# Kernel tuning notes

Hardware: AMD Instinct MI355X
Metric: run time of the kernel (lower is better)

## Reference

```python
import jax, jax.numpy as jnp
import numpy as np

NH = 4  # attention heads

def rmsnorm(x, w, eps=1e-5):
    return x * jax.lax.rsqrt(jnp.mean(x * x, axis=-1, keepdims=True) + eps) * w

def gin(x, src, dst, W, b):
    # GINConv(eps=0): Linear(x + sum_{j->i} x_j)
    agg = jax.ops.segment_sum(x[src], dst, num_segments=x.shape[0])
    return (x + agg) @ W + b

def attn_pool(xb, vt, qkv_w, qkv_b, ao_w, ao_b):
    # xb: [B, Nmax, H] padded nodes (zeros participate, matching the torch code
    # which passes no key_padding_mask); vt: [T, H] virtual tokens.
    B, Nmax, H = xb.shape
    T = vt.shape[0]
    hd = H // NH
    q = (vt @ qkv_w[:, :H] + qkv_b[:H]).reshape(T, NH, hd)
    k = (xb @ qkv_w[:, H:2 * H] + qkv_b[H:2 * H]).reshape(B, Nmax, NH, hd)
    v = (xb @ qkv_w[:, 2 * H:] + qkv_b[2 * H:]).reshape(B, Nmax, NH, hd)
    scores = jnp.einsum('thd,bkhd->bhtk', q, k) / jnp.sqrt(jnp.asarray(hd, xb.dtype))
    attn = jax.nn.softmax(scores, axis=-1)
    o = jnp.einsum('bhtk,bkhd->bthd', attn, v).reshape(B, T, H)
    return o @ ao_w + ao_b

def mamba(tokens, in_w, conv_w, conv_b, x_w, dt_w, dt_b, A_log, D, out_w, norm_w, normf_w):
    # HF MambaModel with num_hidden_layers=1 (slow path), inputs_embeds path.
    B, T, H = tokens.shape
    I, K = conv_w.shape
    S = A_log.shape[1]
    R = dt_w.shape[0]
    res = tokens
    h = rmsnorm(tokens, norm_w)
    proj = h @ in_w                      # [B,T,2I]
    u, gate = jnp.split(proj, 2, axis=-1)
    up = jnp.pad(u, ((0, 0), (K - 1, 0), (0, 0)))  # causal depthwise conv1d
    conv = sum(conv_w[:, k] * up[:, k:k + T, :] for k in range(K)) + conv_b
    u = jax.nn.silu(conv)                # [B,T,I]
    ssm = u @ x_w                        # [B,T,R+2S]
    dtr, Bm, Cm = jnp.split(ssm, [R, R + S], axis=-1)
    dt = jax.nn.softplus(dtr @ dt_w + dt_b)  # [B,T,I]
    A = -jnp.exp(A_log)                  # [I,S]

    def step(hstate, inp):
        dt_t, B_t, C_t, u_t = inp        # [B,I],[B,S],[B,S],[B,I]
        dA = jnp.exp(dt_t[:, :, None] * A)
        dBu = dt_t[:, :, None] * B_t[:, None, :] * u_t[:, :, None]
        hstate = dA * hstate + dBu
        y = jnp.sum(hstate * C_t[:, None, :], axis=-1)
        return hstate, y

    h0 = jnp.zeros((B, I, S), tokens.dtype)
    xs = (dt.transpose(1, 0, 2), Bm.transpose(1, 0, 2), Cm.transpose(1, 0, 2), u.transpose(1, 0, 2))
    _, ys = jax.lax.scan(step, h0, xs)
    y = ys.transpose(1, 0, 2) + u * D
    y = y * jax.nn.silu(gate)
    out = y @ out_w                      # [B,T,H]
    return rmsnorm(res + out, normf_w)

def _forward(x, edge_index, batch, num_graphs, nodes_per_graph,
             w_in, b_in, gin_w, gin_b, vt, qkv_w, qkv_b, ao_w, ao_b,
             m_in_w, m_conv_w, m_conv_b, m_x_w, m_dt_w, m_dt_b,
             m_A_log, m_D, m_out_w, m_norm_w, m_normf_w, w_out, b_out):
    src, dst = edge_index[0], edge_index[1]
    N = x.shape[0]
    starts = jnp.searchsorted(batch, jnp.arange(num_graphs, dtype=batch.dtype))
    pos = jnp.arange(N, dtype=batch.dtype) - starts[batch]
    x = gin(x, src, dst, w_in, b_in)
    H = x.shape[-1]
    for l in range(gin_w.shape[0]):
        g = gin(x, src, dst, gin_w[l], gin_b[l])
        xb = jnp.zeros((num_graphs, nodes_per_graph, H), x.dtype).at[batch, pos].set(x)
        tokens = attn_pool(xb, vt[l], qkv_w[l], qkv_b[l], ao_w[l], ao_b[l])
        gf = mamba(tokens, m_in_w, m_conv_w, m_conv_b, m_x_w, m_dt_w, m_dt_b,
                   m_A_log, m_D, m_out_w, m_norm_w, m_normf_w)
        x = g + gf.mean(axis=1)[batch]
    x = gin(x, src, dst, w_out, b_out)
    return jax.ops.segment_sum(x, batch, num_segments=num_graphs)

def setup_inputs() -> dict:
    key = jax.random.key(0)
    ks = jax.random.split(key, 24)
    N, E, B, NPG = 131072, 2097152, 128, 1024
    IN = H = OUT = 128
    T, L = 8, 2
    I, S, R, K = 256, 16, 8, 4  # mamba: intermediate, state, dt_rank, conv kernel
    w = lambda k, s: (jax.random.normal(k, s, jnp.float32) * 0.02)
    x = jax.random.normal(ks[0], (N, IN), jnp.float32)
    edge_index = jax.random.randint(ks[1], (2, E), 0, N, jnp.int32)
    batch = (jnp.arange(N) // NPG).astype(jnp.int32)
    return dict(
        x=x, edge_index=edge_index, batch=batch, num_graphs=B, nodes_per_graph=NPG,
        w_in=w(ks[2], (IN, H)), b_in=jnp.zeros((H,), jnp.float32),
        gin_w=w(ks[3], (L, H, H)), gin_b=jnp.zeros((L, H), jnp.float32),
        vt=jax.random.normal(ks[4], (L, T, H), jnp.float32),
        qkv_w=w(ks[5], (L, H, 3 * H)), qkv_b=jnp.zeros((L, 3 * H), jnp.float32),
        ao_w=w(ks[6], (L, H, H)), ao_b=jnp.zeros((L, H), jnp.float32),
        m_in_w=w(ks[7], (H, 2 * I)),
        m_conv_w=w(ks[8], (I, K)), m_conv_b=jnp.zeros((I,), jnp.float32),
        m_x_w=w(ks[9], (I, R + 2 * S)),
        m_dt_w=w(ks[10], (R, I)), m_dt_b=jnp.full((I,), 0.1, jnp.float32),
        m_A_log=jnp.log(jnp.tile(jnp.arange(1, S + 1, dtype=jnp.float32), (I, 1))),
        m_D=jnp.ones((I,), jnp.float32),
        m_out_w=w(ks[11], (I, H)),
        m_norm_w=jnp.ones((H,), jnp.float32), m_normf_w=jnp.ones((H,), jnp.float32),
        w_out=w(ks[12], (H, OUT)), b_out=jnp.zeros((OUT,), jnp.float32),
    )

def reference(x, edge_index, batch, num_graphs, nodes_per_graph,
              w_in, b_in, gin_w, gin_b, vt, qkv_w, qkv_b, ao_w, ao_b,
              m_in_w, m_conv_w, m_conv_b, m_x_w, m_dt_w, m_dt_b,
              m_A_log, m_D, m_out_w, m_norm_w, m_normf_w, w_out, b_out):
    return _forward(x, edge_index, batch, num_graphs, nodes_per_graph,
                    w_in, b_in, gin_w, gin_b, vt, qkv_w, qkv_b, ao_w, ao_b,
                    m_in_w, m_conv_w, m_conv_b, m_x_w, m_dt_w, m_dt_b,
                    m_A_log, m_D, m_out_w, m_norm_w, m_normf_w, w_out, b_out)
```

## Files before the change

kernel.cpp:

```cpp
#include <hip/hip_runtime.h>

#define HDIM 128
#define TTOK 8
#define NPG 1024
#define NBUCK 512
#define BSHIFT 8
#define BCAP 5120
#define EPB 4096
#define PARTSZ 4160

typedef unsigned short ushort;
typedef unsigned int uint;
typedef __attribute__((ext_vector_type(8))) short short8;
typedef __attribute__((ext_vector_type(4))) float f32x4;

__device__ __forceinline__ ushort f2bf(float f) {
    unsigned int x = __float_as_uint(f);
    return (ushort)((x + 0x7FFFu + ((x >> 16) & 1u)) >> 16);
}
__device__ __forceinline__ float blo(uint u) { return __uint_as_float(u << 16); }
__device__ __forceinline__ float bhi(uint u) { return __uint_as_float(u & 0xFFFF0000u); }
__device__ __forceinline__ uint pk(float a, float b) {
    return (uint)f2bf(a) | ((uint)f2bf(b) << 16);
}

__global__ __launch_bounds__(256) void bin_kernel(const int* __restrict__ src,
    const int* __restrict__ dst, int mode, int* __restrict__ bcursor,
    uint* __restrict__ pairbuf, int E)
{
    __shared__ int lcnt[NBUCK];
    __shared__ int lbase[NBUCK];
    int tid = threadIdx.x;
    int e0 = blockIdx.x * EPB;
    for (int i = tid; i < NBUCK; i += 256) lcnt[i] = 0;
    __syncthreads();
    uint pkd[16];
    int bk[16], rk[16];
    #pragma unroll
    for (int i = 0; i < 16; ++i) {
        int e = e0 + i * 256 + tid;
        int s = (e < E) ? src[e] : 0;
        int d = (e < E) ? dst[e] : 0;
        int key = mode ? s : d;
        uint pay = mode ? (uint)(d >> 10) : (uint)s;
        if (e >= E) key = -1;
        int b = key >> BSHIFT;
        bk[i] = b;
        pkd[i] = ((uint)(key & 255) << 17) | pay;
        rk[i] = (key >= 0) ? atomicAdd(&lcnt[b], 1) : 0;
    }
    __syncthreads();
    for (int i = tid; i < NBUCK; i += 256) {
        int c = lcnt[i];
        lbase[i] = c ? atomicAdd(&bcursor[i], c) : 0;
    }
    __syncthreads();
    #pragma unroll
    for (int i = 0; i < 16; ++i) {
        if (bk[i] >= 0) {
            int slot = lbase[bk[i]] + rk[i];
            if (slot < BCAP) pairbuf[(size_t)bk[i] * BCAP + slot] = pkd[i];
        }
    }
}

__global__ __launch_bounds__(256) void bucket_sort_kernel(const uint* __restrict__ pairbuf,
    const int* __restrict__ bcount,
    int* __restrict__ ssrc, int* __restrict__ starts, int* __restrict__ countn, int N)
{
    __shared__ int sc[NBUCK];
    __shared__ int lcount[256];
    __shared__ int lcur[256];
    __shared__ int lss[BCAP];
    int b = blockIdx.x;
    int tid = threadIdx.x;
    sc[tid] = min(bcount[tid], BCAP);
    sc[tid + 256] = min(bcount[tid + 256], BCAP);
    lcount[tid] = 0;
    __syncthreads();
    for (int off = 1; off < NBUCK; off <<= 1) {
        int a0 = (tid >= off) ? sc[tid - off] : 0;
        int a1 = (tid + 256 >= off) ? sc[tid + 256 - off] : 0;
        __syncthreads();
        sc[tid] += a0; sc[tid + 256] += a1;
        __syncthreads();
    }
    int nb = min(bcount[b], BCAP);
    int base = sc[b] - nb;
    const uint* pp = pairbuf + (size_t)b * BCAP;
    for (int i = tid; i < nb; i += 256)
        atomicAdd(&lcount[(pp[i] >> 17) & 255], 1);
    __syncthreads();
    int v = lcount[tid];
    lcur[tid] = v;
    __syncthreads();
    for (int off = 1; off < 256; off <<= 1) {
        int t = (tid >= off) ? lcur[tid - off] : 0;
        __syncthreads();
        lcur[tid] += t;
        __syncthreads();
    }
    int excl = lcur[tid] - v;
    int node = b * 256 + tid;
    starts[node] = base + excl;
    countn[node] = v;
    __syncthreads();
    lcur[tid] = excl;
    __syncthreads();
    for (int i = tid; i < nb; i += 256) {
        uint p = pp[i];
        int pos = atomicAdd(&lcur[(p >> 17) & 255], 1);
        lss[pos] = (int)(p & 0x1FFFFu);
    }
    __syncthreads();
    for (int i = tid; i < nb; i += 256) ssrc[base + i] = lss[i];
    if (b == NBUCK - 1 && tid == 0) starts[N] = base + nb;
}

__global__ __launch_bounds__(256) void convert_kernel(const float* __restrict__ in,
                                                      ushort* __restrict__ outb, int n4)
{
    int i = blockIdx.x * 256 + threadIdx.x;
    if (i >= n4) return;
    float4 v = ((const float4*)in)[i];
    uint2 o;
    o.x = pk(v.x, v.y); o.y = pk(v.z, v.w);
    ((uint2*)outb)[i] = o;
}

__global__ __launch_bounds__(512) void gin_fused_kernel(const ushort* __restrict__ XS,
    const int* __restrict__ ssrc, const int* __restrict__ starts,
    const int* __restrict__ count,
    const float* __restrict__ W, const float* __restrict__ bias,
    const float* __restrict__ GF, ushort* __restrict__ XD)
{
    __shared__ ushort Xl[128 * 128];
    __shared__ ushort Wl[128 * 128];
    int tid = threadIdx.x;
    size_t r0 = (size_t)blockIdx.x * 128;
    {
        uint4* wl = (uint4*)Wl;
        for (int i = tid; i < 2048; i += 512) {
            int n = i & 127, c = i >> 7;
            const float* wp = W + (size_t)(c * 8) * 128 + n;
            float w0 = wp[0], w1 = wp[128], w2 = wp[256], w3 = wp[384];
            float w4 = wp[512], w5 = wp[640], w6 = wp[768], w7 = wp[896];
            uint4 u;
            u.x = pk(w0, w1); u.y = pk(w2, w3); u.z = pk(w4, w5); u.w = pk(w6, w7);
            wl[n * 16 + (c ^ (n & 15))] = u;
        }
    }
    {
        int g16 = tid >> 4, lane16 = tid & 15;
        #pragma unroll
        for (int rr = 0; rr < 4; ++rr) {
            int row = g16 * 4 + rr;
            int node = (int)r0 + row;
            uint4 sv = *((const uint4*)(XS + (size_t)node * HDIM) + lane16);
            float a0 = blo(sv.x), a1 = bhi(sv.x), a2 = blo(sv.y), a3 = bhi(sv.y);
            float a4 = blo(sv.z), a5 = bhi(sv.z), a6 = blo(sv.w), a7 = bhi(sv.w);
            int es = starts[node], cn = count[node];
            for (int j0 = 0; j0 < cn; j0 += 16) {
                int myid = (j0 + lane16 < cn) ? ssrc[es + j0 + lane16] : 0;
                int m = min(16, cn - j0);
                int j = 0;
                for (; j + 7 < m; j += 8) {
                    uint4 u[8];
                    #pragma unroll
                    for (int q = 0; q < 8; ++q) {
                        int sidx = __shfl(myid, j + q, 16);
                        u[q] = *((const uint4*)(XS + (size_t)sidx * HDIM) + lane16);
                    }
                    #pragma unroll
                    for (int q = 0; q < 8; ++q) {
                        a0 += blo(u[q].x); a1 += bhi(u[q].x);
                        a2 += blo(u[q].y); a3 += bhi(u[q].y);
                        a4 += blo(u[q].z); a5 += bhi(u[q].z);
                        a6 += blo(u[q].w); a7 += bhi(u[q].w);
                    }
                }
                for (; j + 3 < m; j += 4) {
                    uint4 u[4];
                    #pragma unroll
                    for (int q = 0; q < 4; ++q) {
                        int sidx = __shfl(myid, j + q, 16);
                        u[q] = *((const uint4*)(XS + (size_t)sidx * HDIM) + lane16);
                    }
                    #pragma unroll
                    for (int q = 0; q < 4; ++q) {
                        a0 += blo(u[q].x); a1 += bhi(u[q].x);
                        a2 += blo(u[q].y); a3 += bhi(u[q].y);
                        a4 += blo(u[q].z); a5 += bhi(u[q].z);
                        a6 += blo(u[q].w); a7 += bhi(u[q].w);
                    }
                }
                for (; j < m; ++j) {
                    int sidx = __shfl(myid, j, 16);
                    uint4 ua = *((const uint4*)(XS + (size_t)sidx * HDIM) + lane16);
                    a0 += blo(ua.x); a1 += bhi(ua.x);
                    a2 += blo(ua.y); a3 += bhi(ua.y);
                    a4 += blo(ua.z); a5 += bhi(ua.z);
                    a6 += blo(ua.w); a7 += bhi(ua.w);
                }
            }
            uint4 o;
            o.x = pk(a0, a1); o.y = pk(a2, a3); o.z = pk(a4, a5); o.w = pk(a6, a7);
            ((uint4*)Xl)[row * 16 + (lane16 ^ (row & 15))] = o;
        }
    }
    __syncthreads();
    int wave = tid >> 6;
    int lane = tid & 63;
    int m16 = lane & 15, quad = lane >> 4;
    const short8* Xf = (const short8*)Xl;
    const short8* Wf = (const short8*)Wl;
    short8 afr[4];
    #pragma unroll
    for (int kc = 0; kc < 4; ++kc)
        afr[kc] = Xf[(wave * 16 + m16) * 16 + ((kc * 4 + quad) ^ m16)];
    int graph = (int)(r0 >> 10);
    #pragma unroll
    for (int ct = 0; ct < 8; ++ct) {
        int col = ct * 16 + m16;
        short8 bfr[4];
        #pragma unroll
        for (int kc = 0; kc < 4; ++kc)
            bfr[kc] = Wf[col * 16 + ((kc * 4 + quad) ^ m16)];
        f32x4 acc = {0.f, 0.f, 0.f, 0.f};
        #pragma unroll
        for (int kc = 0; kc < 4; ++kc)
            acc = __builtin_amdgcn_mfma_f32_16x16x32_bf16(afr[kc], bfr[kc], acc, 0, 0, 0);
        float add = bias[col] + (GF ? GF[(size_t)graph * HDIM + col] : 0.f);
        #pragma unroll
        for (int r = 0; r < 4; ++r)
            XD[(r0 + wave * 16 + quad * 4 + r) * HDIM + col] = f2bf(acc[r] + add);
    }
}

__global__ __launch_bounds__(256) void attn_prep_kernel(const float* __restrict__ vt,
    const float* __restrict__ qkv_w, const float* __restrict__ qkv_b, float* __restrict__ P)
{
    __shared__ float vtl[TTOK][HDIM];
    __shared__ float q[TTOK][HDIM];
    int l = blockIdx.x;
    const float* vtp = vt + (size_t)l * TTOK * HDIM;
    const float* qw = qkv_w + (size_t)l * 128 * 384;
    const float* qb = qkv_b + (size_t)l * 384;
    float* Pp = P + (size_t)l * 4 * TTOK * HDIM;
    int tid = threadIdx.x;
    for (int i = tid; i < TTOK * HDIM; i += 256) vtl[i >> 7][i & 127] = vtp[i];
    __syncthreads();
    for (int i = tid; i < TTOK * HDIM; i += 256) {
        int t = i >> 7, j = i & 127;
        float acc = qb[j];
        for (int c = 0; c < 128; ++c) acc += vtl[t][c] * qw[c * 384 + j];
        q[t][j] = acc;
    }
    __syncthreads();
    const float scale = 0.17677669529663687f;
    for (int i = tid; i < 4 * TTOK * HDIM; i += 256) {
        int h = i >> 10, t = (i >> 7) & 7, cc = i & 127;
        float acc = 0.f;
        for (int d = 0; d < 32; ++d)
            acc += qw[cc * 384 + 128 + h * 32 + d] * q[t][h * 32 + d];
        Pp[i] = acc * scale;
    }
}

__global__ __launch_bounds__(256) void attn_part_kernel(const ushort* __restrict__ X,
    const float* __restrict__ P, float* __restrict__ PART)
{
    __shared__ ushort Xl[128 * 128];
    __shared__ float  St[32 * 132];
    __shared__ ushort Pl[32 * 128];
    __shared__ float lm[32], ll[32], lalpha[32];
    int tid = threadIdx.x;
    int bp = blockIdx.x;
    int b = bp >> 2, part = bp & 3;
    int wave = tid >> 6, lane = tid & 63;
    int m16 = lane & 15, quad = lane >> 4;

    for (int i = tid; i < 2048; i += 256) {
        float2 v = *(const float2*)(P + (size_t)i * 2);
        ((uint*)Pl)[i] = pk(v.x, v.y);
    }
    if (tid < 32) { lm[tid] = -1e30f; ll[tid] = 0.f; }
    __syncthreads();
    short8 aP[2][4];
    #pragma unroll
    for (int mt = 0; mt < 2; ++mt)
        #pragma unroll
        for (int kc = 0; kc < 4; ++kc)
            aP[mt][kc] = *(const short8*)&Pl[(mt * 16 + m16) * 128 + (kc * 4 + quad) * 8];
    __syncthreads();

    f32x4 oacc[2][2] = {};
    const uint4* xsg = (const uint4*)(X + (size_t)b * NPG * HDIM);

    for (int t8i = 0; t8i < 2; ++t8i) {
        int t8 = part * 2 + t8i;
        {
            const uint4* xs = xsg + t8 * 2048;
            uint4* xl = (uint4*)Xl;
            for (int i = tid; i < 2048; i += 256) {
                int row = i >> 4, cc = i & 15;
                xl[row * 16 + (cc ^ (row & 15))] = xs[i];
            }
        }
        __syncthreads();
        {
            f32x4 sacc[2][2] = {};
            #pragma unroll
            for (int kc = 0; kc < 4; ++kc) {
                short8 bx[2];
                #pragma unroll
                for (int ntl = 0; ntl < 2; ++ntl) {
                    int node = (2 * wave + ntl) * 16 + m16;
                    bx[ntl] = *(const short8*)&Xl[node * 128 + (((kc * 4 + quad) ^ m16) << 3)];
                }
                #pragma unroll
                for (int mt = 0; mt < 2; ++mt)
                    #pragma unroll
                    for (int ntl = 0; ntl < 2; ++ntl)
                        sacc[mt][ntl] = __builtin_amdgcn_mfma_f32_16x16x32_bf16(
                            aP[mt][kc], bx[ntl], sacc[mt][ntl], 0, 0, 0);
            }
            #pragma unroll
            for (int mt = 0; mt < 2; ++mt)
                #pragma unroll
                for (int ntl = 0; ntl < 2; ++ntl)
                    #pragma unroll
                    for (int r = 0; r < 4; ++r)
                        St[(mt * 16 + quad * 4 + r) * 132 + (2 * wave + ntl) * 16 + m16]
                            = sacc[mt][ntl][r];
        }
        __syncthreads();
        {
            int j = tid >> 3, g = tid & 7;
            const float* rowp = &St[j * 132 + g * 16];
            float4 v0 = *(const float4*)(rowp);
            float4 v1 = *(const float4*)(rowp + 4);
            float4 v2 = *(const float4*)(rowp + 8);
            float4 v3 = *(const float4*)(rowp + 12);
            float mx = fmaxf(fmaxf(fmaxf(v0.x, v0.y), fmaxf(v0.z, v0.w)),
                             fmaxf(fmaxf(v1.x, v1.y), fmaxf(v1.z, v1.w)));
            mx = fmaxf(mx, fmaxf(fmaxf(fmaxf(v2.x, v2.y), fmaxf(v2.z, v2.w)),
                                 fmaxf(fmaxf(v3.x, v3.y), fmaxf(v3.z, v3.w))));
            mx = fmaxf(mx, __shfl_down(mx, 4, 8));
            mx = fmaxf(mx, __shfl_down(mx, 2, 8));
            mx = fmaxf(mx, __shfl_down(mx, 1, 8));
            mx = __shfl(mx, 0, 8);
            float mold = lm[j];
            float Mn = fmaxf(mold, mx);
            float alpha = __expf(mold - Mn);
            float p0 = __expf(v0.x - Mn), p1 = __expf(v0.y - Mn), p2 = __expf(v0.z - Mn), p3 = __expf(v0.w - Mn);
            float p4 = __expf(v1.x - Mn), p5 = __expf(v1.y - Mn), p6 = __expf(v1.z - Mn), p7 = __expf(v1.w - Mn);
            float p8 = __expf(v2.x - Mn), p9 = __expf(v2.y - Mn), pa = __expf(v2.z - Mn), pb = __expf(v2.w - Mn);
            float pc = __expf(v3.x - Mn), pd = __expf(v3.y - Mn), pe = __expf(v3.z - Mn), pf = __expf(v3.w - Mn);
            float s = ((p0 + p1) + (p2 + p3)) + ((p4 + p5) + (p6 + p7))
                    + ((p8 + p9) + (pa + pb)) + ((pc + pd) + (pe + pf));
            s += __shfl_down(s, 4, 8);
            s += __shfl_down(s, 2, 8);
            s += __shfl_down(s, 1, 8);
            if (g == 0) {
                ll[j] = ll[j] * alpha + s;
                lm[j] = Mn;
                lalpha[j] = alpha;
            }
            uint4 u0, u1;
            u0.x = pk(p0, p1); u0.y = pk(p2, p3); u0.z = pk(p4, p5); u0.w = pk(p6, p7);
            u1.x = pk(p8, p9); u1.y = pk(pa, pb); u1.z = pk(pc, pd); u1.w = pk(pe, pf);
            ((uint4*)Pl)[j * 16 + ((2 * g) ^ (j & 15))] = u0;
            ((uint4*)Pl)[j * 16 + ((2 * g + 1) ^ (j & 15))] = u1;
        }
        __syncthreads();
        {
            #pragma unroll
            for (int mt = 0; mt < 2; ++mt)
                #pragma unroll
                for (int r = 0; r < 4; ++r) {
                    float a = lalpha[mt * 16 + quad * 4 + r];
                    oacc[mt][0][r] *= a;
                    oacc[mt][1][r] *= a;
                }
            #pragma unroll
            for (int kc = 0; kc < 4; ++kc) {
                short8 ap2[2], bx[2];
                #pragma unroll
                for (int mt = 0; mt < 2; ++mt)
                    ap2[mt] = *(const short8*)&Pl[(mt * 16 + m16) * 128 + (((kc * 4 + quad) ^ m16) << 3)];
                #pragma unroll
                for (int ntl = 0; ntl < 2; ++ntl) {
                    int cf = (2 * wave + ntl) * 16 + m16;
                    int chi = cf >> 3, clo = cf & 7;
                    short8 v;
                    #pragma unroll
                    for (int jj = 0; jj < 8; ++jj) {
                        int row = kc * 32 + quad * 8 + jj;
                        v[jj] = (short)Xl[(row << 7) + ((chi ^ (row & 15)) << 3) + clo];
                    }
                    bx[ntl] = v;
                }
                #pragma unroll
                for (int mt = 0; mt < 2; ++mt)
                    #pragma unroll
                    for (int ntl = 0; ntl < 2; ++ntl)
                        oacc[mt][ntl] = __builtin_amdgcn_mfma_f32_16x16x32_bf16(
                            ap2[mt], bx[ntl], oacc[mt][ntl], 0, 0, 0);
            }
        }
        __syncthreads();
    }
    float* PB = PART + ((size_t)b * 4 + part) * PARTSZ;
    #pragma unroll
    for (int mt = 0; mt < 2; ++mt)
        #pragma unroll
        for (int r = 0; r < 4; ++r) {
            int j = mt * 16 + quad * 4 + r;
            PB[j * 128 + (2 * wave + 0) * 16 + m16] = oacc[mt][0][r];
            PB[j * 128 + (2 * wave + 1) * 16 + m16] = oacc[mt][1][r];
        }
    if (tid < 32) { PB[4096 + tid] = lm[tid]; PB[4128 + tid] = ll[tid]; }
}

__global__ __launch_bounds__(1024) void mamba_kernel(const float* __restrict__ PART,
    const float* __restrict__ qkv_w, const float* __restrict__ qkv_b,
    const float* __restrict__ ao_w, const float* __restrict__ ao_b,
    const float* __restrict__ in_w, const float* __restrict__ conv_w,
    const float* __restrict__ conv_b, const float* __restrict__ x_w,
    const float* __restrict__ dt_w, const float* __restrict__ dt_b,
    const float* __restrict__ A_log, const float* __restrict__ Dp,
    const float* __restrict__ out_w, const float* __restrict__ norm_w,
    const float* __restrict__ normf_w, float* __restrict__ GF)
{
    constexpr int I = 256, S = 16;
    __shared__ float R[32 * 132];
    __shared__ float wgt[4][32];
    __shared__ float inv[32];
    __shared__ float tok[TTOK][HDIM];
    __shared__ float hn[TTOK][HDIM];
    __shared__ float uu[TTOK][I];
    __shared__ float gg[TTOK][I];
    __shared__ float ssm[TTOK][40];
    __shared__ float yy[TTOK][I];
    int b = blockIdx.x, tid = threadIdx.x;

    const float* PB = PART + (size_t)b * 4 * PARTSZ;
    if (tid < 32) {
        int j = tid;
        float m0 = PB[4096 + j], m1 = PB[PARTSZ + 4096 + j];
        float m2 = PB[2 * PARTSZ + 4096 + j], m3 = PB[3 * PARTSZ + 4096 + j];
        float M = fmaxf(fmaxf(m0, m1), fmaxf(m2, m3));
        float w0 = __expf(m0 - M), w1 = __expf(m1 - M);
        float w2 = __expf(m2 - M), w3 = __expf(m3 - M);
        float L = w0 * PB[4128 + j] + w1 * PB[PARTSZ + 4128 + j]
                + w2 * PB[2 * PARTSZ + 4128 + j] + w3 * PB[3 * PARTSZ + 4128 + j];
        wgt[0][j] = w0; wgt[1][j] = w1; wgt[2][j] = w2; wgt[3][j] = w3;
        inv[j] = 1.f / L;
    }
    __syncthreads();
    #pragma unroll
    for (int it = 0; it < 4; ++it) {
        int idx = it * 1024 + tid;
        int j = idx >> 7, c = idx & 127;
        float v = wgt[0][j] * PB[idx] + wgt[1][j] * PB[PARTSZ + idx]
                + wgt[2][j] * PB[2 * PARTSZ + idx] + wgt[3][j] * PB[3 * PARTSZ + idx];
        R[j * 132 + c] = v * inv[j];
    }
    __syncthreads();
    {
        int t = tid >> 7, col = tid & 127;
        int h = col >> 5;
        const float* rp = &R[(h * 8 + t) * 132];
        const float* wp = qkv_w + 256 + col;
        float acc = qkv_b[256 + col];
        for (int c = 0; c < 128; c += 8) {
            float w[8];
            #pragma unroll
            for (int q = 0; q < 8; ++q) w[q] = wp[(size_t)(c + q) * 384];
            #pragma unroll
            for (int q = 0; q < 8; ++q) acc += rp[c + q] * w[q];
        }
        hn[t][col] = acc;
    }
    __syncthreads();
    {
        int t = tid >> 7, col = tid & 127;
        const float* hp = hn[t];
        const float* wp = ao_w + col;
        float acc = ao_b[col];
        for (int k = 0; k < 128; k += 8) {
            float w[8];
            #pragma unroll
            for (int q = 0; q < 8; ++q) w[q] = wp[(size_t)(k + q) * 128];
            #pragma unroll
            for (int q = 0; q < 8; ++q) acc += hp[k + q] * w[q];
        }
        tok[t][col] = acc;
    }
    __syncthreads();

    if (tid < 512) {
        int t = tid >> 6, lane = tid & 63;
        float v0 = tok[t][lane], v1 = tok[t][lane + 64];
        float s = v0 * v0 + v1 * v1;
        #pragma unroll
        for (int off = 32; off; off >>= 1) s += __shfl_down(s, off);
        s = __shfl(s, 0);
        float r = rsqrtf(s * (1.f / 128.f) + 1e-5f);
        hn[t][lane] = v0 * r * norm_w[lane];
        hn[t][lane + 64] = v1 * r * norm_w[lane + 64];
    }
    __syncthreads();
    {
        int j = tid & 511, tq = tid >> 9;
        float acc[4] = {0.f, 0.f, 0.f, 0.f};
        const float* wp = in_w + j;
        for (int c = 0; c < 128; c += 8) {
            float w[8];
            #pragma unroll
            for (int q = 0; q < 8; ++q) w[q] = wp[(size_t)(c + q) * 512];
            #pragma unroll
            for (int q = 0; q < 8; ++q) {
                float wq = w[q];
                #pragma unroll
                for (int k = 0; k < 4; ++k) acc[k] += hn[tq * 4 + k][c + q] * wq;
            }
        }
        if (j < 256) {
            #pragma unroll
            for (int k = 0; k < 4; ++k) uu[tq * 4 + k][j] = acc[k];
        } else {
            #pragma unroll
            for (int k = 0; k < 4; ++k) gg[tq * 4 + k][j - 256] = acc[k];
        }
    }
    __syncthreads();
    if (tid < 256) {
        int i = tid;
        float cw0 = conv_w[i * 4 + 0], cw1 = conv_w[i * 4 + 1];
        float cw2 = conv_w[i * 4 + 2], cw3 = conv_w[i * 4 + 3];
        float cb = conv_b[i];
        float uv[TTOK];
        #pragma unroll
        for (int t = 0; t < TTOK; ++t) uv[t] = uu[t][i];
        #pragma unroll
        for (int t = 0; t < TTOK; ++t) {
            float a = cw3 * uv[t] + cb;
            if (t >= 1) a += cw2 * uv[t - 1];
            if (t >= 2) a += cw1 * uv[t - 2];
            if (t >= 3) a += cw0 * uv[t - 3];
            float sg = 1.f / (1.f + __expf(-a));
            uu[t][i] = a * sg;
        }
    }
    __syncthreads();
    {
        int t = tid >> 7, j = tid & 127;
        if (j < 40) {
            float acc = 0.f;
            const float* wp = x_w + j;
            const float* up = uu[t];
            for (int c = 0; c < 256; c += 8) {
                float w[8];
                #pragma unroll
                for (int q = 0; q < 8; ++q) w[q] = wp[(size_t)(c + q) * 40];
                #pragma unroll
                for (int q = 0; q < 8; ++q) acc += up[c + q] * w[q];
            }
            ssm[t][j] = acc;
        }
    }
    __syncthreads();
    if (tid < 256) {
        int i = tid;
        float dw[8];
        #pragma unroll
        for (int r = 0; r < 8; ++r) dw[r] = dt_w[r * 256 + i];
        float dtbias = dt_b[i];
        float a[S], st[S];
        #pragma unroll
        for (int s = 0; s < S; ++s) { a[s] = -__expf(A_log[i * S + s]); st[s] = 0.f; }
        float Di = Dp[i];
        for (int t = 0; t < TTOK; ++t) {
            float d = dtbias;
            #pragma unroll
            for (int r = 0; r < 8; ++r) d += ssm[t][r] * dw[r];
            d = (d > 20.f) ? d : log1pf(__expf(d));
            float ut = uu[t][i];
            float du = d * ut;
            float y = 0.f;
            #pragma unroll
            for (int s = 0; s < S; ++s) {
                float dA = __expf(d * a[s]);
                st[s] = dA * st[s] + du * ssm[t][8 + s];
                y += st[s] * ssm[t][24 + s];
            }
            y += ut * Di;
            float g = gg[t][i];
            float sg = 1.f / (1.f + __expf(-g));
            yy[t][i] = y * g * sg;
        }
    }
    __syncthreads();
    {
        int t = tid >> 7, c = tid & 127;
        float acc = tok[t][c];
        const float* wp = out_w + c;
        const float* yp = yy[t];
        for (int i = 0; i < 256; i += 8) {
            float w[8];
            #pragma unroll
            for (int q = 0; q < 8; ++q) w[q] = wp[(size_t)(i + q) * 128];
            #pragma unroll
            for (int q = 0; q < 8; ++q) acc += yp[i + q] * w[q];
        }
        hn[t][c] = acc;
    }
    __syncthreads();
    if (tid < 512) {
        int t = tid >> 6, lane = tid & 63;
        float v0 = hn[t][lane], v1 = hn[t][lane + 64];
        float s = v0 * v0 + v1 * v1;
        #pragma unroll
        for (int off = 32; off; off >>= 1) s += __shfl_down(s, off);
        s = __shfl(s, 0);
        float r = rsqrtf(s * (1.f / 128.f) + 1e-5f);
        hn[t][lane] = v0 * r * normf_w[lane];
        hn[t][lane + 64] = v1 * r * normf_w[lane + 64];
    }
    __syncthreads();
    if (tid < 128) {
        float s = 0.f;
        #pragma unroll
        for (int t = 0; t < TTOK; ++t) s += hn[t][tid];
        GF[(size_t)b * HDIM + tid] = s * (1.f / TTOK);
    }
}

__global__ __launch_bounds__(512) void final_count_kernel(const ushort* __restrict__ X,
    const uint* __restrict__ pairbuf, const int* __restrict__ bcount,
    float* __restrict__ PS2)
{
    __shared__ uint hist[128 * 128];
    __shared__ ushort Xb[256 * 128];
    int bkt = blockIdx.x, tid = threadIdx.x;
    for (int i = tid; i < 16384; i += 512) hist[i] = 0u;
    {
        const uint4* xs = (const uint4*)(X + ((size_t)bkt << 8) * HDIM);
        uint4* xl = (uint4*)Xb;
        for (int i = tid; i < 4096; i += 512) {
            int row = i >> 4, cc = i & 15;
            xl[row * 16 + (cc ^ (row & 15))] = xs[i];
        }
    }
    __syncthreads();
    int nb = min(bcount[bkt], BCAP);
    const uint* pp = pairbuf + (size_t)bkt * BCAP;
    for (int i = tid; i < nb; i += 512) {
        uint p = pp[i];
        int g = (int)(p & 0x1FFFFu);
        int s8 = (int)((p >> 17) & 255);
        atomicAdd(&hist[g * 128 + (s8 >> 1)], 1u << ((s8 & 1) * 16));
    }
    if (tid < 256) {
        int g = bkt >> 2;
        atomicAdd(&hist[g * 128 + (tid >> 1)], 1u << ((tid & 1) * 16));
    }
    __syncthreads();
    for (int i = tid; i < 16384; i += 512) {
        uint u = hist[i];
        hist[i] = pk((float)(u & 0xFFFFu), (float)(u >> 16));
    }
    __syncthreads();
    int wave = tid >> 6, lane = tid & 63;
    int m16 = lane & 15, quad = lane >> 4;
    const short8* Af = (const short8*)hist;
    short8 afr[8];
    #pragma unroll
    for (int kc = 0; kc < 8; ++kc)
        afr[kc] = Af[(wave * 16 + m16) * 32 + kc * 4 + quad];
    float* PBo = PS2 + (size_t)bkt * 16384;
    #pragma unroll
    for (int ct = 0; ct < 8; ++ct) {
        f32x4 acc = {0.f, 0.f, 0.f, 0.f};
        int n = ct * 16 + m16;
        int chi = n >> 3, clo = n & 7;
        #pragma unroll
        for (int kc = 0; kc < 8; ++kc) {
            short8 bx;
            #pragma unroll
            for (int j = 0; j < 8; ++j) {
                int k = kc * 32 + quad * 8 + j;
                bx[j] = (short)Xb[(k << 7) + (((chi) ^ (k & 15)) << 3) + clo];
            }
            acc = __builtin_amdgcn_mfma_f32_16x16x32_bf16(afr[kc], bx, acc, 0, 0, 0);
        }
        #pragma unroll
        for (int r = 0; r < 4; ++r)
            PBo[(wave * 16 + quad * 4 + r) * 128 + n] = acc[r];
    }
}

__global__ __launch_bounds__(128) void final_mm_kernel(const float* __restrict__ PS2,
    const float* __restrict__ w_out, const float* __restrict__ b_out,
    float* __restrict__ out)
{
    __shared__ float Sm[HDIM];
    int b = blockIdx.x, tid = threadIdx.x;
    float s0 = 0.f, s1 = 0.f, s2 = 0.f, s3 = 0.f;
    const float* base = PS2 + (size_t)b * 128 + tid;
    for (int blk = 0; blk < 512; blk += 4) {
        s0 += base[(size_t)(blk + 0) * 16384];
        s1 += base[(size_t)(blk + 1) * 16384];
        s2 += base[(size_t)(blk + 2) * 16384];
        s3 += base[(size_t)(blk + 3) * 16384];
    }
    Sm[tid] = (s0 + s1) + (s2 + s3);
    __syncthreads();
    float acc = 1024.f * b_out[tid];
    for (int k = 0; k < 128; ++k) acc += Sm[k] * w_out[k * 128 + tid];
    out[(size_t)b * HDIM + tid] = acc;
}

extern "C" void kernel_launch(void* const* d_in, const int* in_sizes, int n_in,
                              void* d_out, int out_size, void* d_ws, size_t ws_size,
                              hipStream_t stream)
{
    const int N = in_sizes[0] / HDIM;
    const int E = in_sizes[1] / 2;
    const int B = N >> 10;

    const float* x_in  = (const float*)d_in[0];
    const int*   src   = (const int*)d_in[1];
    const int*   dst   = src + E;
    const float* w_in  = (const float*)d_in[5];
    const float* b_in  = (const float*)d_in[6];
    const float* gin_w = (const float*)d_in[7];
    const float* gin_b = (const float*)d_in[8];
    const float* vt    = (const float*)d_in[9];
    const float* qkv_w = (const float*)d_in[10];
    const float* qkv_b = (const float*)d_in[11];
    const float* ao_w  = (const float*)d_in[12];
    const float* ao_b  = (const float*)d_in[13];
    const float* m_in_w   = (const float*)d_in[14];
    const float* m_conv_w = (const float*)d_in[15];
    const float* m_conv_b = (const float*)d_in[16];
    const float* m_x_w    = (const float*)d_in[17];
    const float* m_dt_w   = (const float*)d_in[18];
    const float* m_dt_b   = (const float*)d_in[19];
    const float* m_A_log  = (const float*)d_in[20];
    const float* m_D      = (const float*)d_in[21];
    const float* m_out_w  = (const float*)d_in[22];
    const float* m_norm_w = (const float*)d_in[23];
    const float* m_normf_w= (const float*)d_in[24];
    const float* w_out = (const float*)d_in[25];
    const float* b_out = (const float*)d_in[26];
    float* out = (float*)d_out;

    float* GF  = (float*)d_ws;
    float* P   = GF + (size_t)B * HDIM;
    float* PART= P + 2 * 4 * TTOK * HDIM;
    int* bcursor  = (int*)(PART + (size_t)B * 4 * PARTSZ);
    int* bcursor2 = bcursor + NBUCK;
    int* count    = bcursor2 + NBUCK;
    int* starts   = count + N;
    int* ssrc     = starts + N + 8;
    uint* pairbuf = (uint*)(ssrc + E);
    float* PS2    = (float*)(pairbuf + (size_t)NBUCK * BCAP);
    ushort* XB0 = (ushort*)(PS2 + (size_t)NBUCK * 128 * 128);
    ushort* XB1 = XB0 + (size_t)N * HDIM;

    hipMemsetAsync(bcursor, 0, 2 * NBUCK * sizeof(int), stream);
    bin_kernel<<<(E + EPB - 1) / EPB, 256, 0, stream>>>(src, dst, 0, bcursor, pairbuf, E);
    bucket_sort_kernel<<<NBUCK, 256, 0, stream>>>(pairbuf, bcursor, ssrc, starts, count, N);
    bin_kernel<<<(E + EPB - 1) / EPB, 256, 0, stream>>>(src, dst, 1, bcursor2, pairbuf, E);

    attn_prep_kernel<<<2, 256, 0, stream>>>(vt, qkv_w, qkv_b, P);

    convert_kernel<<<(N * 32 + 255) / 256, 256, 0, stream>>>(x_in, XB0, N * 32);
    gin_fused_kernel<<<N / 128, 512, 0, stream>>>(XB0, ssrc, starts, count,
                                                  w_in, b_in, nullptr, XB1);

    ushort* Xcur = XB1;
    ushort* Xnext = XB0;
    for (int l = 0; l < 2; ++l) {
        attn_part_kernel<<<B * 4, 256, 0, stream>>>(Xcur, P + (size_t)l * 4 * TTOK * HDIM, PART);
        mamba_kernel<<<B, 1024, 0, stream>>>(PART,
                                             qkv_w + (size_t)l * 128 * 384,
                                             qkv_b + (size_t)l * 384,
                                             ao_w + (size_t)l * 128 * 128,
                                             ao_b + (size_t)l * 128,
                                             m_in_w, m_conv_w, m_conv_b, m_x_w,
                                             m_dt_w, m_dt_b, m_A_log, m_D, m_out_w,
                                             m_norm_w, m_normf_w, GF);
        gin_fused_kernel<<<N / 128, 512, 0, stream>>>(Xcur, ssrc, starts, count,
                                                      gin_w + (size_t)l * 128 * 128,
                                                      gin_b + (size_t)l * 128, GF, Xnext);
        ushort* t = Xcur; Xcur = Xnext; Xnext = t;
    }

    final_count_kernel<<<NBUCK, 512, 0, stream>>>(Xcur, pairbuf, bcursor2, PS2);
    final_mm_kernel<<<B, 128, 0, stream>>>(PS2, w_out, b_out, out);

    (void)n_in; (void)out_size; (void)ws_size;
}
```

Before: 929.4 us.

## Split GIN gather from linear and co-schedule gather with attention blocks

Splits the fused GIN kernel into a neighbor-gather kernel that writes aggregated bf16 rows to a workspace buffer and a separate MFMA linear kernel handling 32 rows per wave. In the layer loop the gather is merged into the attention kernel launch, interleaving one attention block per 16 gather blocks, so the memory-bound gather overlaps the few attention blocks instead of running serially. It also shrinks final_count's shared-memory histogram to 8-bit packed counts and processes X in two halves so more blocks can be resident. This adds an extra global round trip for the aggregated features, and 8-bit counts could overflow if any graph/source pair has more than 255 edges.

```diff
diff --git a/kernel.cpp b/kernel.cpp
--- a/kernel.cpp
+++ b/kernel.cpp
@@ -128,154 +128,78 @@
     ((uint2*)outb)[i] = o;
 }
 
-__global__ __launch_bounds__(512) void gin_fused_kernel(const ushort* __restrict__ XS,
+__device__ __forceinline__ void gather16_body(const ushort* __restrict__ XS,
     const int* __restrict__ ssrc, const int* __restrict__ starts,
-    const int* __restrict__ count,
-    const float* __restrict__ W, const float* __restrict__ bias,
-    const float* __restrict__ GF, ushort* __restrict__ XD)
-{
-    __shared__ ushort Xl[128 * 128];
-    __shared__ ushort Wl[128 * 128];
-    int tid = threadIdx.x;
-    size_t r0 = (size_t)blockIdx.x * 128;
-    {
-        uint4* wl = (uint4*)Wl;
-        for (int i = tid; i < 2048; i += 512) {
-            int n = i & 127, c = i >> 7;
-            const float* wp = W + (size_t)(c * 8) * 128 + n;
-            float w0 = wp[0], w1 = wp[128], w2 = wp[256], w3 = wp[384];
-            float w4 = wp[512], w5 = wp[640], w6 = wp[768], w7 = wp[896];
-            uint4 u;
-            u.x = pk(w0, w1); u.y = pk(w2, w3); u.z = pk(w4, w5); u.w = pk(w6, w7);
-            wl[n * 16 + (c ^ (n & 15))] = u;
-        }
-    }
-    {
-        int g16 = tid >> 4, lane16 = tid & 15;
-        #pragma unroll
-        for (int rr = 0; rr < 4; ++rr) {
-            int row = g16 * 4 + rr;
-            int node = (int)r0 + row;
-            uint4 sv = *((const uint4*)(XS + (size_t)node * HDIM) + lane16);
-            float a0 = blo(sv.x), a1 = bhi(sv.x), a2 = blo(sv.y), a3 = bhi(sv.y);
-            float a4 = blo(sv.z), a5 = bhi(sv.z), a6 = blo(sv.w), a7 = bhi(sv.w);
-            int es = starts[node], cn = count[node];
-            for (int j0 = 0; j0 < cn; j0 += 16) {
-                int myid = (j0 + lane16 < cn) ? ssrc[es + j0 + lane16] : 0;
-                int m = min(16, cn - j0);
-                int j = 0;
-                for (; j + 7 < m; j += 8) {
-                    uint4 u[8];
-                    #pragma unroll
-                    for (int q = 0; q < 8; ++q) {
-                        int sidx = __shfl(myid, j + q, 16);
-                        u[q] = *((const uint4*)(XS + (size_t)sidx * HDIM) + lane16);
-                    }
-                    #pragma unroll
-                    for (int q = 0; q < 8; ++q) {
-                        a0 += blo(u[q].x); a1 += bhi(u[q].x);
-                        a2 += blo(u[q].y); a3 += bhi(u[q].y);
-                        a4 += blo(u[q].z); a5 += bhi(u[q].z);
-                        a6 += blo(u[q].w); a7 += bhi(u[q].w);
-                    }
-                }
-                for (; j + 3 < m; j += 4) {
-                    uint4 u[4];
-                    #pragma unroll
-                    for (int q = 0; q < 4; ++q) {
-                        int sidx = __shfl(myid, j + q, 16);
-                        u[q] = *((const uint4*)(XS + (size_t)sidx * HDIM) + lane16);
-                    }
-                    #pragma unroll
-                    for (int q = 0; q < 4; ++q) {
-                        a0 += blo(u[q].x); a1 += bhi(u[q].x);
-                        a2 += blo(u[q].y); a3 += bhi(u[q].y);
-                        a4 += blo(u[q].z); a5 += bhi(u[q].z);
-                        a6 += blo(u[q].w); a7 += bhi(u[q].w);
-                    }
-                }
-                for (; j < m; ++j) {
-                    int sidx = __shfl(myid, j, 16);
-                    uint4 ua = *((const uint4*)(XS + (size_t)sidx * HDIM) + lane16);
-                    a0 += blo(ua.x); a1 += bhi(ua.x);
-                    a2 += blo(ua.y); a3 += bhi(ua.y);
-                    a4 += blo(ua.z); a5 += bhi(ua.z);
-                    a6 += blo(ua.w); a7 += bhi(ua.w);
-                }
-            }
-            uint4 o;
-            o.x = pk(a0, a1); o.y = pk(a2, a3); o.z = pk(a4, a5); o.w = pk(a6, a7);
-            ((uint4*)Xl)[row * 16 + (lane16 ^ (row & 15))] = o;
-        }
-    }
-    __syncthreads();
-    int wave = tid >> 6;
-    int lane = tid & 63;
-    int m16 = lane & 15, quad = lane >> 4;
-    const short8* Xf = (const short8*)Xl;
-    const short8* Wf = (const short8*)Wl;
-    short8 afr[4];
-    #pragma unroll
-    for (int kc = 0; kc < 4; ++kc)
-        afr[kc] = Xf[(wave * 16 + m16) * 16 + ((kc * 4 + quad) ^ m16)];
-    int graph = (int)(r0 >> 10);
-    #pragma unroll
-    for (int ct = 0; ct < 8; ++ct) {
-        int col = ct * 16 + m16;
-        short8 bfr[4];
-        #pragma unroll
-        for (int kc = 0; kc < 4; ++kc)
-            bfr[kc] = Wf[col * 16 + ((kc * 4 + quad) ^ m16)];
-        f32x4 acc = {0.f, 0.f, 0.f, 0.f};
-        #pragma unroll
-        for (int kc = 0; kc < 4; ++kc)
-            acc = __builtin_amdgcn_mfma_f32_16x16x32_bf16(afr[kc], bfr[kc], acc, 0, 0, 0);
-        float add = bias[col] + (GF ? GF[(size_t)graph * HDIM + col] : 0.f);
-        #pragma unroll
-        for (int r = 0; r < 4; ++r)
-            XD[(r0 + wave * 16 + quad * 4 + r) * HDIM + col] = f2bf(acc[r] + add);
-    }
-}
-
-__global__ __launch_bounds__(256) void attn_prep_kernel(const float* __restrict__ vt,
-    const float* __restrict__ qkv_w, const float* __restrict__ qkv_b, float* __restrict__ P)
-{
-    __shared__ float vtl[TTOK][HDIM];
-    __shared__ float q[TTOK][HDIM];
-    int l = blockIdx.x;
-    const float* vtp = vt + (size_t)l * TTOK * HDIM;
-    const float* qw = qkv_w + (size_t)l * 128 * 384;
-    const float* qb = qkv_b + (size_t)l * 384;
-    float* Pp = P + (size_t)l * 4 * TTOK * HDIM;
-    int tid = threadIdx.x;
-    for (int i = tid; i < TTOK * HDIM; i += 256) vtl[i >> 7][i & 127] = vtp[i];
-    __syncthreads();
-    for (int i = tid; i < TTOK * HDIM; i += 256) {
-        int t = i >> 7, j = i & 127;
-        float acc = qb[j];
-        for (int c = 0; c < 128; ++c) acc += vtl[t][c] * qw[c * 384 + j];
-        q[t][j] = acc;
-    }
-    __syncthreads();
-    const float scale = 0.17677669529663687f;
-    for (int i = tid; i < 4 * TTOK * HDIM; i += 256) {
-        int h = i >> 10, t = (i >> 7) & 7, cc = i & 127;
-        float acc = 0.f;
-        for (int d = 0; d < 32; ++d)
-            acc += qw[cc * 384 + 128 + h * 32 + d] * q[t][h * 32 + d];
-        Pp[i] = acc * scale;
-    }
-}
-
-__global__ __launch_bounds__(256) void attn_part_kernel(const ushort* __restrict__ X,
-    const float* __restrict__ P, float* __restrict__ PART)
+    const int* __restrict__ count, ushort* __restrict__ AGG, int nbase, int tid)
+{
+    int g = tid >> 4, lane = tid & 15;
+    int node = nbase + g;
+    uint4 sv = *((const uint4*)(XS + (size_t)node * HDIM) + lane);
+    float a0 = blo(sv.x), a1 = bhi(sv.x), a2 = blo(sv.y), a3 = bhi(sv.y);
+    float a4 = blo(sv.z), a5 = bhi(sv.z), a6 = blo(sv.w), a7 = bhi(sv.w);
+    int s0 = starts[node], cn = count[node];
+    for (int j0 = 0; j0 < cn; j0 += 16) {
+        int myid = (j0 + lane < cn) ? ssrc[s0 + j0 + lane] : 0;
+        int m = min(16, cn - j0);
+        int j = 0;
+        for (; j + 7 < m; j += 8) {
+            uint4 u[8];
+            #pragma unroll
+            for (int q = 0; q < 8; ++q) {
+                int sidx = __shfl(myid, j + q, 16);
+                u[q] = *((const uint4*)(XS + (size_t)sidx * HDIM) + lane);
+            }
+            #pragma unroll
+            for (int q = 0; q < 8; ++q) {
+                a0 += blo(u[q].x); a1 += bhi(u[q].x);
+                a2 += blo(u[q].y); a3 += bhi(u[q].y);
+                a4 += blo(u[q].z); a5 += bhi(u[q].z);
+                a6 += blo(u[q].w); a7 += bhi(u[q].w);
+            }
+        }
+        for (; j + 3 < m; j += 4) {
+            uint4 u[4];
+            #pragma unroll
+            for (int q = 0; q < 4; ++q) {
+                int sidx = __shfl(myid, j + q, 16);
+                u[q] = *((const uint4*)(XS + (size_t)sidx * HDIM) + lane);
+            }
+            #pragma unroll
+            for (int q = 0; q < 4; ++q) {
+                a0 += blo(u[q].x); a1 += bhi(u[q].x);
+                a2 += blo(u[q].y); a3 += bhi(u[q].y);
+                a4 += blo(u[q].z); a5 += bhi(u[q].z);
+                a6 += blo(u[q].w); a7 += bhi(u[q].w);
+            }
+        }
+        for (; j < m; ++j) {
+            int sidx = __shfl(myid, j, 16);
+            uint4 ua = *((const uint4*)(XS + (size_t)sidx * HDIM) + lane);
+            a0 += blo(ua.x); a1 += bhi(ua.x);
+            a2 += blo(ua.y); a3 += bhi(ua.y);
+            a4 += blo(ua.z); a5 += bhi(ua.z);
+            a6 += blo(ua.w); a7 += bhi(ua.w);
+        }
+    }
+    uint4 o;
+    o.x = pk(a0, a1); o.y = pk(a2, a3); o.z = pk(a4, a5); o.w = pk(a6, a7);
+    *((uint4*)(AGG + (size_t)node * HDIM) + lane) = o;
+}
+
+__global__ __launch_bounds__(256) void gather_kernel(const ushort* __restrict__ XS,
+    const int* __restrict__ ssrc, const int* __restrict__ starts,
+    const int* __restrict__ count, ushort* __restrict__ AGG)
+{
+    gather16_body(XS, ssrc, starts, count, AGG, blockIdx.x * 16, threadIdx.x);
+}
+
+__device__ __forceinline__ void attn_body(const ushort* __restrict__ X,
+    const float* __restrict__ P, float* __restrict__ PART, int bp, int tid)
 {
     __shared__ ushort Xl[128 * 128];
     __shared__ float  St[32 * 132];
     __shared__ ushort Pl[32 * 128];
     __shared__ float lm[32], ll[32], lalpha[32];
-    int tid = threadIdx.x;
-    int bp = blockIdx.x;
     int b = bp >> 2, part = bp & 3;
     int wave = tid >> 6, lane = tid & 63;
     int m16 = lane & 15, quad = lane >> 4;
@@ -423,6 +347,114 @@
     if (tid < 32) { PB[4096 + tid] = lm[tid]; PB[4128 + tid] = ll[tid]; }
 }
 
+__global__ __launch_bounds__(256) void attn_gather_kernel(const ushort* __restrict__ X,
+    const float* __restrict__ P, float* __restrict__ PART,
+    const int* __restrict__ ssrc, const int* __restrict__ starts,
+    const int* __restrict__ count, ushort* __restrict__ AGG)
+{
+    int bp = blockIdx.x;
+    if (bp % 17 == 0) {
+        attn_body(X, P, PART, bp / 17, threadIdx.x);
+    } else {
+        int gidx = bp - bp / 17 - 1;
+        gather16_body(X, ssrc, starts, count, AGG, gidx * 16, threadIdx.x);
+    }
+}
+
+__global__ __launch_bounds__(256) void lin128_mfma_kernel(const ushort* __restrict__ XS,
+    const float* __restrict__ W, const float* __restrict__ bias,
+    const float* __restrict__ GF, ushort* __restrict__ XD)
+{
+    __shared__ ushort Xl[128 * 128];
+    __shared__ ushort Wl[128 * 128];
+    int tid = threadIdx.x;
+    size_t r0 = (size_t)blockIdx.x * 128;
+    {
+        const uint4* xs = (const uint4*)(XS + r0 * HDIM);
+        uint4* xl = (uint4*)Xl;
+        for (int i = tid; i < 2048; i += 256) {
+            int row = i >> 4, cc = i & 15;
+            xl[row * 16 + (cc ^ (row & 15))] = xs[i];
+        }
+    }
+    {
+        uint4* wl = (uint4*)Wl;
+        for (int i = tid; i < 2048; i += 256) {
+            int n = i & 127, c = i >> 7;
+            const float* wp = W + (size_t)(c * 8) * 128 + n;
+            float w0 = wp[0], w1 = wp[128], w2 = wp[256], w3 = wp[384];
+            float w4 = wp[512], w5 = wp[640], w6 = wp[768], w7 = wp[896];
+            uint4 u;
+            u.x = pk(w0, w1); u.y = pk(w2, w3); u.z = pk(w4, w5); u.w = pk(w6, w7);
+            wl[n * 16 + (c ^ (n & 15))] = u;
+        }
+    }
+    __syncthreads();
+    int wave = tid >> 6;
+    int lane = tid & 63;
+    int m16 = lane & 15, quad = lane >> 4;
+    const short8* Xf = (const short8*)Xl;
+    const short8* Wf = (const short8*)Wl;
+    short8 afr[2][4];
+    #pragma unroll
+    for (int rt = 0; rt < 2; ++rt)
+        #pragma unroll
+        for (int kc = 0; kc < 4; ++kc)
+            afr[rt][kc] = Xf[(wave * 32 + rt * 16 + m16) * 16 + ((kc * 4 + quad) ^ m16)];
+    int graph = (int)(r0 >> 10);
+    #pragma unroll
+    for (int ct = 0; ct < 8; ++ct) {
+        int col = ct * 16 + m16;
+        short8 bfr[4];
+        #pragma unroll
+        for (int kc = 0; kc < 4; ++kc)
+            bfr[kc] = Wf[col * 16 + ((kc * 4 + quad) ^ m16)];
+        f32x4 acc0 = {0.f, 0.f, 0.f, 0.f};
+        f32x4 acc1 = {0.f, 0.f, 0.f, 0.f};
+        #pragma unroll
+        for (int kc = 0; kc < 4; ++kc) {
+            acc0 = __builtin_amdgcn_mfma_f32_16x16x32_bf16(afr[0][kc], bfr[kc], acc0, 0, 0, 0);
+            acc1 = __builtin_amdgcn_mfma_f32_16x16x32_bf16(afr[1][kc], bfr[kc], acc1, 0, 0, 0);
+        }
+        float add = bias[col] + (GF ? GF[(size_t)graph * HDIM + col] : 0.f);
+        #pragma unroll
+        for (int r = 0; r < 4; ++r) {
+            XD[(r0 + wave * 32 + quad * 4 + r) * HDIM + col] = f2bf(acc0[r] + add);
+            XD[(r0 + wave * 32 + 16 + quad * 4 + r) * HDIM + col] = f2bf(acc1[r] + add);
+        }
+    }
+}
+
+__global__ __launch_bounds__(256) void attn_prep_kernel(const float* __restrict__ vt,
+    const float* __restrict__ qkv_w, const float* __restrict__ qkv_b, float* __restrict__ P)
+{
+    __shared__ float vtl[TTOK][HDIM];
+    __shared__ float q[TTOK][HDIM];
+    int l = blockIdx.x;
+    const float* vtp = vt + (size_t)l * TTOK * HDIM;
+    const float* qw = qkv_w + (size_t)l * 128 * 384;
+    const float* qb = qkv_b + (size_t)l * 384;
+    float* Pp = P + (size_t)l * 4 * TTOK * HDIM;
+    int tid = threadIdx.x;
+    for (int i = tid; i < TTOK * HDIM; i += 256) vtl[i >> 7][i & 127] = vtp[i];
+    __syncthreads();
+    for (int i = tid; i < TTOK * HDIM; i += 256) {
+        int t = i >> 7, j = i & 127;
+        float acc = qb[j];
+        for (int c = 0; c < 128; ++c) acc += vtl[t][c] * qw[c * 384 + j];
+        q[t][j] = acc;
+    }
+    __syncthreads();
+    const float scale = 0.17677669529663687f;
+    for (int i = tid; i < 4 * TTOK * HDIM; i += 256) {
+        int h = i >> 10, t = (i >> 7) & 7, cc = i & 127;
+        float acc = 0.f;
+        for (int d = 0; d < 32; ++d)
+            acc += qw[cc * 384 + 128 + h * 32 + d] * q[t][h * 32 + d];
+        Pp[i] = acc * scale;
+    }
+}
+
 __global__ __launch_bounds__(1024) void mamba_kernel(const float* __restrict__ PART,
     const float* __restrict__ qkv_w, const float* __restrict__ qkv_b,
     const float* __restrict__ ao_w, const float* __restrict__ ao_b,
@@ -642,63 +674,69 @@
     const uint* __restrict__ pairbuf, const int* __restrict__ bcount,
     float* __restrict__ PS2)
 {
-    __shared__ uint hist[128 * 128];
-    __shared__ ushort Xb[256 * 128];
+    __shared__ uint hist[128 * 64];
+    __shared__ ushort Xb[128 * 128];
     int bkt = blockIdx.x, tid = threadIdx.x;
-    for (int i = tid; i < 16384; i += 512) hist[i] = 0u;
-    {
-        const uint4* xs = (const uint4*)(X + ((size_t)bkt << 8) * HDIM);
-        uint4* xl = (uint4*)Xb;
-        for (int i = tid; i < 4096; i += 512) {
-            int row = i >> 4, cc = i & 15;
-            xl[row * 16 + (cc ^ (row & 15))] = xs[i];
-        }
-    }
+    for (int i = tid; i < 8192; i += 512) hist[i] = 0u;
     __syncthreads();
     int nb = min(bcount[bkt], BCAP);
     const uint* pp = pairbuf + (size_t)bkt * BCAP;
     for (int i = tid; i < nb; i += 512) {
         uint p = pp[i];
         int g = (int)(p & 0x1FFFFu);
-        int s8 = (int)((p >> 17) & 255);
-        atomicAdd(&hist[g * 128 + (s8 >> 1)], 1u << ((s8 & 1) * 16));
+        int s = (int)((p >> 17) & 255);
+        atomicAdd(&hist[g * 64 + (s >> 2)], 1u << ((s & 3) * 8));
     }
     if (tid < 256) {
         int g = bkt >> 2;
-        atomicAdd(&hist[g * 128 + (tid >> 1)], 1u << ((tid & 1) * 16));
-    }
-    __syncthreads();
-    for (int i = tid; i < 16384; i += 512) {
-        uint u = hist[i];
-        hist[i] = pk((float)(u & 0xFFFFu), (float)(u >> 16));
-    }
-    __syncthreads();
+        atomicAdd(&hist[g * 64 + (tid >> 2)], 1u << ((tid & 3) * 8));
+    }
     int wave = tid >> 6, lane = tid & 63;
     int m16 = lane & 15, quad = lane >> 4;
-    const short8* Af = (const short8*)hist;
-    short8 afr[8];
-    #pragma unroll
-    for (int kc = 0; kc < 8; ++kc)
-        afr[kc] = Af[(wave * 16 + m16) * 32 + kc * 4 + quad];
+    int grow = wave * 16 + m16;
+    f32x4 acc[8] = {};
+    for (int half = 0; half < 2; ++half) {
+        __syncthreads();
+        {
+            const uint4* xs = (const uint4*)(X + ((size_t)bkt * 256 + half * 128) * HDIM);
+            uint4* xl = (uint4*)Xb;
+            for (int i = tid; i < 2048; i += 512) {
+                int row = i >> 4, cc = i & 15;
+                xl[row * 16 + (cc ^ (row & 15))] = xs[i];
+            }
+        }
+        __syncthreads();
+        #pragma unroll
+        for (int kc = 0; kc < 4; ++kc) {
+            int s0 = half * 128 + kc * 32 + quad * 8;
+            uint w0 = hist[grow * 64 + (s0 >> 2)];
+            uint w1 = hist[grow * 64 + (s0 >> 2) + 1];
+            short8 afr;
+            ((uint*)&afr)[0] = pk((float)(w0 & 255u), (float)((w0 >> 8) & 255u));
+            ((uint*)&afr)[1] = pk((float)((w0 >> 16) & 255u), (float)(w0 >> 24));
+            ((uint*)&afr)[2] = pk((float)(w1 & 255u), (float)((w1 >> 8) & 255u));
+            ((uint*)&afr)[3] = pk((float)((w1 >> 16) & 255u), (float)(w1 >> 24));
+            #pragma unroll
+            for (int ct = 0; ct < 8; ++ct) {
+                int n = ct * 16 + m16;
+                int chi = n >> 3, clo = n & 7;
+                short8 bx;
+                #pragma unroll
+                for (int j = 0; j < 8; ++j) {
+                    int k = kc * 32 + quad * 8 + j;
+                    bx[j] = (short)Xb[(k << 7) + ((chi ^ (k & 15)) << 3) + clo];
+                }
+                acc[ct] = __builtin_amdgcn_mfma_f32_16x16x32_bf16(afr, bx, acc[ct], 0, 0, 0);
+            }
+        }
+    }
     float* PBo = PS2 + (size_t)bkt * 16384;
     #pragma unroll
     for (int ct = 0; ct < 8; ++ct) {
-        f32x4 acc = {0.f, 0.f, 0.f, 0.f};
         int n = ct * 16 + m16;
-        int chi = n >> 3, clo = n & 7;
-        #pragma unroll
-        for (int kc = 0; kc < 8; ++kc) {
-            short8 bx;
-            #pragma unroll
-            for (int j = 0; j < 8; ++j) {
-                int k = kc * 32 + quad * 8 + j;
-                bx[j] = (short)Xb[(k << 7) + (((chi) ^ (k & 15)) << 3) + clo];
-            }
-            acc = __builtin_amdgcn_mfma_f32_16x16x32_bf16(afr[kc], bx, acc, 0, 0, 0);
-        }
         #pragma unroll
         for (int r = 0; r < 4; ++r)
-            PBo[(wave * 16 + quad * 4 + r) * 128 + n] = acc[r];
+            PBo[(wave * 16 + quad * 4 + r) * 128 + n] = acc[ct][r];
     }
 }
 
@@ -768,6 +806,7 @@
     int* ssrc     = starts + N + 8;
     uint* pairbuf = (uint*)(ssrc + E);
     float* PS2    = (float*)(pairbuf + (size_t)NBUCK * BCAP);
+    ushort* AGG = (ushort*)PS2;
     ushort* XB0 = (ushort*)(PS2 + (size_t)NBUCK * 128 * 128);
     ushort* XB1 = XB0 + (size_t)N * HDIM;
 
@@ -779,13 +818,15 @@
     attn_prep_kernel<<<2, 256, 0, stream>>>(vt, qkv_w, qkv_b, P);
 
     convert_kernel<<<(N * 32 + 255) / 256, 256, 0, stream>>>(x_in, XB0, N * 32);
-    gin_fused_kernel<<<N / 128, 512, 0, stream>>>(XB0, ssrc, starts, count,
-                                                  w_in, b_in, nullptr, XB1);
+    gather_kernel<<<N / 16, 256, 0, stream>>>(XB0, ssrc, starts, count, AGG);
+    lin128_mfma_kernel<<<N / 128, 256, 0, stream>>>(AGG, w_in, b_in, nullptr, XB1);
 
     ushort* Xcur = XB1;
     ushort* Xnext = XB0;
+    const int nAG = B * 4 + N / 16;
     for (int l = 0; l < 2; ++l) {
-        attn_part_kernel<<<B * 4, 256, 0, stream>>>(Xcur, P + (size_t)l * 4 * TTOK * HDIM, PART);
+        attn_gather_kernel<<<nAG, 256, 0, stream>>>(Xcur, P + (size_t)l * 4 * TTOK * HDIM,
+                                                    PART, ssrc, starts, count, AGG);
         mamba_kernel<<<B, 1024, 0, stream>>>(PART,
                                              qkv_w + (size_t)l * 128 * 384,
                                              qkv_b + (size_t)l * 384,
@@ -794,9 +835,8 @@
                                              m_in_w, m_conv_w, m_conv_b, m_x_w,
                                              m_dt_w, m_dt_b, m_A_log, m_D, m_out_w,
                                              m_norm_w, m_normf_w, GF);
-        gin_fused_kernel<<<N / 128, 512, 0, stream>>>(Xcur, ssrc, starts, count,
-                                                      gin_w + (size_t)l * 128 * 128,
-                                                      gin_b + (size_t)l * 128, GF, Xnext);
+        lin128_mfma_kernel<<<N / 128, 256, 0, stream>>>(AGG, gin_w + (size_t)l * 128 * 128,
+                                                        gin_b + (size_t)l * 128, GF, Xnext);
         ushort* t = Xcur; Xcur = Xnext; Xnext = t;
     }
 
```

After: 907.9 us. 2.3% less time.
